# Performance work log

Measured on AMD Instinct MI355X. Metric: run time of the kernel, lower is better.

Reference implementation:

```python
import jax, jax.numpy as jnp
import numpy as np

BIG = 1e8  # > max possible squared distance in a 64^3 volume (3*63^2 ~ 1.2e4)


def _edt(mask):
    """Exact Euclidean distance transform (scipy.ndimage.distance_transform_edt).

    mask: [B, X, Y, Z] float; distance at nonzero voxels to nearest zero voxel.
    Uses the exact separable squared-EDT: along each axis,
      g[i] = min_j f[j] + (i - j)^2  (lower envelope of parabolas, brute-forced).
    """
    f = jnp.where(mask > 0, BIG, 0.0).astype(jnp.float32)
    for ax in (1, 2, 3):
        f = jnp.moveaxis(f, ax, -1)            # [..., n]
        n = f.shape[-1]
        i = jnp.arange(n)
        d2 = ((i[:, None] - i[None, :]) ** 2).astype(jnp.float32)  # [n, n]
        f = jnp.min(f[..., None, :] + d2, axis=-1)                 # [..., n]
        f = jnp.moveaxis(f, -1, ax)
    return jnp.sqrt(f)


def _get_dist_map(mmap, label_inner, label_outer):
    lz = jnp.isin(mmap, jnp.asarray(label_outer)).astype(jnp.float32)
    lz = jnp.where(jnp.isin(mmap, jnp.asarray(label_inner)), 0.0, lz)
    tdm_outer = _edt(lz)                       # distance inside outer region to its zero set
    b = _edt(1.0 - lz)
    boundary = jnp.where(b == 1.0, 1.0, 0.0)   # boundary[boundary != 1] = 0
    outer = tdm_outer + boundary
    level_zero_inner = (outer == 0.0).astype(jnp.float32)
    tsd = -_edt(level_zero_inner) + tdm_outer  # signed distance
    return boundary, tsd


def setup_inputs() -> dict:
    key = jax.random.key(0)
    mmap = jax.random.randint(key, (2, 64, 64, 64), 0, 10, dtype=jnp.int32)
    return {"mmap": mmap}


def reference(mmap):
    d_mean = 2.0
    inner_boundary, phi_inner = _get_dist_map(mmap, [3, 5, 6, 7, 8, 9], [2, 1, 4, 0])
    outer_boundary, phi_outer = _get_dist_map(mmap, [3, 5, 6, 7, 8, 9, 2], [1, 4, 0])
    hausdorff_inner = jnp.abs(inner_boundary * phi_outer)
    hausdorff_outer = jnp.abs(outer_boundary * phi_inner)
    h_in_mean = hausdorff_inner.sum() / inner_boundary.sum()
    h_out_mean = hausdorff_outer.sum() / outer_boundary.sum()
    loss = (h_in_mean - d_mean) ** 2 + (h_out_mean - d_mean) ** 2
    return (h_in_mean, hausdorff_inner.max(), h_out_mean, hausdorff_outer.max(), loss)
```

## Files before the change

### kernel.cpp

```cpp
#include <hip/hip_runtime.h>
#include <math.h>

#define N 64
#define PLANE 4096
#define FBIG 3.4e38f
#define MASK1 0x17u
#define MASK2 0x13u
typedef unsigned long long ull;

#define PART_OFF ((size_t)131072)
#define CTR_OFF (PART_OFF + (size_t)256 * 8 * 4)

__global__ __launch_bounds__(512) void build_bits(const int* __restrict__ mmap,
                                                  void* __restrict__ wsv) {
  __shared__ unsigned char colb[2][8][64];
  const int bid = blockIdx.x;
  const int b = bid >> 6, x = bid & 63;
  const int t = threadIdx.x;
  const int z = t & 63, c = t >> 6;
  const size_t pb = (size_t)(b * N + x) * PLANE;
  unsigned b1 = 0, b2 = 0;
  #pragma unroll
  for (int k = 0; k < 8; ++k) {
    const int v = mmap[pb + (8 * c + k) * N + z];
    b1 |= ((MASK1 >> v) & 1u) << k;
    b2 |= ((MASK2 >> v) & 1u) << k;
  }
  colb[0][c][z] = (unsigned char)b1;
  colb[1][c][z] = (unsigned char)b2;
  __syncthreads();
  if (t < 128) {
    const int mm = t >> 6, zz = t & 63;
    ull v = 0;
    #pragma unroll
    for (int cc = 0; cc < 8; ++cc)
      v |= (ull)colb[mm][cc][zz] << (8 * cc);
    ((ull*)wsv)[((size_t)(mm * 2 + b) * 64 + x) * 64 + zz] = v;
  }
}

__global__ __launch_bounds__(512) void edt_all(void* __restrict__ wsv,
                                               float* __restrict__ out) {
  __shared__ unsigned int g1p[64][65];
  __shared__ float g2T[64][65];
  __shared__ float g2L[64][65];
  __shared__ unsigned char bndB[4096];
  __shared__ float redS[8], redB[8], redM[8];
  __shared__ int lastFlag;
  const int bid = blockIdx.x;
  const int m = bid >> 7;
  const int y0 = bid & 63;
  const int t = threadIdx.x;

  const ull* cxO = (const ull*)wsv + ((size_t)(bid >> 6) & 3) * 4096;
  const ull* cxP = (const ull*)wsv + (size_t)(((1 - m) * 2) + ((bid >> 6) & 1)) * 4096;

  #pragma unroll
  for (int k = 0; k < 8; ++k) {
    const int ci = t + 512 * k;
    const int x = ci >> 6, z = ci & 63;
    const ull c0 = cxO[ci];
    const ull xm = (x > 0) ? cxO[ci - 64] : 0ull;
    const ull xp = (x < 63) ? cxO[ci + 64] : 0ull;
    const ull zm = (z > 0) ? cxO[ci - 1] : 0ull;
    const ull zp = (z < 63) ? cxO[ci + 1] : 0ull;
    const ull mT = ~c0;
    const ull nb = xm | xp | zm | zp | (c0 << 1) | (c0 >> 1);
    const ull mL = c0 | nb;
    const int zs = z * z;
    unsigned vT, vL;
    {
      const ull hi = mT >> y0;
      const int du = hi ? (__ffsll((long long)hi) - 1) : 99;
      const int dd = (int)__clzll((long long)(mT << (63 - y0)));
      const int d = min(du, dd);
      vT = (d > 63) ? 65535u : (unsigned)(d * d + zs);
    }
    {
      const ull hi = mL >> y0;
      const int du = hi ? (__ffsll((long long)hi) - 1) : 99;
      const int dd = (int)__clzll((long long)(mL << (63 - y0)));
      const int d = min(du, dd);
      vL = (d > 63) ? 65535u : (unsigned)(d * d + zs);
    }
    g1p[x][z] = vT | (vL << 16);
    const ull p0 = cxP[ci];
    const ull pxm = (x > 0) ? cxP[ci - 64] : 0ull;
    const ull pxp = (x < 63) ? cxP[ci + 64] : 0ull;
    const ull pzm = (z > 0) ? cxP[ci - 1] : 0ull;
    const ull pzp = (z < 63) ? cxP[ci + 1] : 0ull;
    const ull pnb = pxm | pxp | pzm | pzp | (p0 << 1) | (p0 >> 1);
    bndB[ci] = (unsigned char)(((pnb & ~p0) >> y0) & 1ull);
  }
  __syncthreads();

  {
    const int x = t >> 3, g = t & 7;
    float aT[8], aL[8], zq[8];
    #pragma unroll
    for (int q = 0; q < 8; ++q) {
      aT[q] = FBIG; aL[q] = FBIG; zq[q] = (float)(g + 8 * q);
    }
    const unsigned* row = &g1p[x][0];
    float m2j = 0.f;
    #pragma unroll 4
    for (int j = 0; j < 64; ++j) {
      const unsigned v = row[j];
      const float fT = (float)(v & 0xffffu);
      const float fL = (float)(v >> 16);
      #pragma unroll
      for (int q = 0; q < 8; ++q) {
        aT[q] = fminf(aT[q], fmaf(m2j, zq[q], fT));
        aL[q] = fminf(aL[q], fmaf(m2j, zq[q], fL));
      }
      m2j -= 2.f;
    }
    const float xs = (float)(x * x);
    #pragma unroll
    for (int q = 0; q < 8; ++q) {
      const int zi = g + 8 * q;
      const float z2 = zq[q] * zq[q];
      g2T[x][zi] = aT[q] + z2 + xs;
      g2L[x][zi] = aL[q] + z2 + xs;
    }
  }
  __syncthreads();

  {
    const int z = t >> 3, g = t & 7;
    float aT[8], aL[8], xq[8];
    #pragma unroll
    for (int q = 0; q < 8; ++q) {
      aT[q] = FBIG; aL[q] = FBIG; xq[q] = (float)(g + 8 * q);
    }
    float m2j = 0.f;
    #pragma unroll 4
    for (int j = 0; j < 64; ++j) {
      const float f1 = g2T[j][z];
      const float f2 = g2L[j][z];
      #pragma unroll
      for (int q = 0; q < 8; ++q) {
        aT[q] = fminf(aT[q], fmaf(m2j, xq[q], f1));
        aL[q] = fminf(aL[q], fmaf(m2j, xq[q], f2));
      }
      m2j -= 2.f;
    }
    float hsum = 0.f, bsum = 0.f, hmax = 0.f;
    #pragma unroll
    for (int q = 0; q < 8; ++q) {
      const int x = g + 8 * q;
      const float eT = fmaf(xq[q], xq[q], aT[q]);
      const float eL = fmaf(xq[q], xq[q], aL[q]);
      const float tsd = sqrtf(eT) - sqrtf(eL);
      const float bnd = (float)bndB[x * 64 + z];
      const float h = bnd * fabsf(tsd);
      hsum += h; bsum += bnd; hmax = fmaxf(hmax, h);
    }
    #pragma unroll
    for (int o = 32; o > 0; o >>= 1) {
      hsum += __shfl_down(hsum, o);
      bsum += __shfl_down(bsum, o);
      hmax = fmaxf(hmax, __shfl_down(hmax, o));
    }
    const int w = t >> 6;
    if ((t & 63) == 0) { redS[w] = hsum; redB[w] = bsum; redM[w] = hmax; }
  }
  __syncthreads();

  float* part = (float*)((char*)wsv + PART_OFF);
  int* ctr = (int*)((char*)wsv + CTR_OFF);
  if (t == 0) {
    float s = 0.f, bs = 0.f, mx = 0.f;
    #pragma unroll
    for (int i = 0; i < 8; ++i) {
      s += redS[i]; bs += redB[i]; mx = fmaxf(mx, redM[i]);
    }
    float* p = part + (size_t)bid * 8;
    p[0] = s; p[1] = bs; p[2] = mx;
    __threadfence();
    const int old = atomicAdd(ctr, 1);
    lastFlag = (old == 255) ? 1 : 0;
  }
  __syncthreads();
  if (lastFlag) {
    __threadfence();
    float s = 0.f, bs = 0.f, mx = 0.f;
    if (t < 256) {
      const float* p = part + (size_t)t * 8;
      s = p[0]; bs = p[1]; mx = p[2];
    }
    #pragma unroll
    for (int o = 32; o > 0; o >>= 1) {
      s += __shfl_down(s, o);
      bs += __shfl_down(bs, o);
      mx = fmaxf(mx, __shfl_down(mx, o));
    }
    __syncthreads();
    if ((t & 63) == 0 && t < 256) {
      redS[t >> 6] = s; redB[t >> 6] = bs; redM[t >> 6] = mx;
    }
    __syncthreads();
    if (t == 0) {
      const float s_ho = redS[0] + redS[1], b2 = redB[0] + redB[1];
      const float mho = fmaxf(redM[0], redM[1]);
      const float s_hi = redS[2] + redS[3], b1 = redB[2] + redB[3];
      const float mhi = fmaxf(redM[2], redM[3]);
      const float him = s_hi / b1;
      const float hom = s_ho / b2;
      out[0] = him;
      out[1] = mhi;
      out[2] = hom;
      out[3] = mho;
      out[4] = (him - 2.f) * (him - 2.f) + (hom - 2.f) * (hom - 2.f);
    }
  }
}

extern "C" void kernel_launch(void* const* d_in, const int* in_sizes, int n_in,
                              void* d_out, int out_size, void* d_ws,
                              size_t ws_size, hipStream_t stream) {
  (void)in_sizes; (void)n_in; (void)out_size; (void)ws_size;
  const int* mmap = (const int*)d_in[0];
  float* out = (float*)d_out;

  hipMemsetAsync((char*)d_ws + CTR_OFF, 0, 8, stream);
  build_bits<<<128, 512, 0, stream>>>(mmap, d_ws);
  edt_all<<<256, 512, 0, stream>>>(d_ws, out);
}
```

Baseline: 37.32 us.

## Precompute stencil masks in separate kernel, pack second pass, use 1024-thread blocks

Adds a stencil kernel that computes the dilated mask and boundary bitmasks once per volume instead of recomputing them in every y-slice block. The second EDT pass now stores packed 16-bit T/L values in a transposed shared array read with 128-bit vector loads. The main kernel doubles its block size to 1024 threads with 4 outputs per thread, reducing per-thread register work. The trade-off is an extra kernel launch and a clamp to 65535 that relies on distances fitting in 16 bits.

Measured after the change: 40.40 us. 1.08x slower.

```diff
diff --git a/kernel.cpp b/kernel.cpp
--- a/kernel.cpp
+++ b/kernel.cpp
@@ -6,9 +6,14 @@
 #define FBIG 3.4e38f
 #define MASK1 0x17u
 #define MASK2 0x13u
+#define LP 68
 typedef unsigned long long ull;
-
-#define PART_OFF ((size_t)131072)
+typedef __attribute__((ext_vector_type(4))) unsigned int u32x4;
+
+#define CX_OFF ((size_t)0)
+#define ML_OFF ((size_t)131072)
+#define BD_OFF ((size_t)262144)
+#define PART_OFF ((size_t)393216)
 #define CTR_OFF (PART_OFF + (size_t)256 * 8 * 4)
 
 __global__ __launch_bounds__(512) void build_bits(const int* __restrict__ mmap,
@@ -35,38 +40,48 @@
     #pragma unroll
     for (int cc = 0; cc < 8; ++cc)
       v |= (ull)colb[mm][cc][zz] << (8 * cc);
-    ((ull*)wsv)[((size_t)(mm * 2 + b) * 64 + x) * 64 + zz] = v;
-  }
-}
-
-__global__ __launch_bounds__(512) void edt_all(void* __restrict__ wsv,
-                                               float* __restrict__ out) {
-  __shared__ unsigned int g1p[64][65];
-  __shared__ float g2T[64][65];
-  __shared__ float g2L[64][65];
-  __shared__ unsigned char bndB[4096];
-  __shared__ float redS[8], redB[8], redM[8];
+    ((ull*)((char*)wsv + CX_OFF))[(size_t)(mm * 2 + b) * 4096 + x * 64 + zz] = v;
+  }
+}
+
+__global__ __launch_bounds__(512) void stencil_k(void* __restrict__ wsv) {
+  const int idx = blockIdx.x * 512 + threadIdx.x;
+  const int mi = idx >> 12, ci = idx & 4095;
+  const int x = ci >> 6, z = ci & 63;
+  const ull* cx = (const ull*)((char*)wsv + CX_OFF) + (size_t)mi * 4096;
+  const ull c0 = cx[ci];
+  const ull xm = (x > 0) ? cx[ci - 64] : 0ull;
+  const ull xp = (x < 63) ? cx[ci + 64] : 0ull;
+  const ull zm = (z > 0) ? cx[ci - 1] : 0ull;
+  const ull zp = (z < 63) ? cx[ci + 1] : 0ull;
+  const ull nb = xm | xp | zm | zp | (c0 << 1) | (c0 >> 1);
+  ((ull*)((char*)wsv + ML_OFF))[(size_t)mi * 4096 + ci] = c0 | nb;
+  ((ull*)((char*)wsv + BD_OFF))[(size_t)mi * 4096 + ci] = nb & ~c0;
+}
+
+__global__ __launch_bounds__(1024) void edt_all(void* __restrict__ wsv,
+                                                float* __restrict__ out) {
+  __shared__ unsigned int g1p[64][LP];
+  __shared__ unsigned int g2p[64][LP];
+  __shared__ float redS[16], redB[16], redM[16];
   __shared__ int lastFlag;
   const int bid = blockIdx.x;
   const int m = bid >> 7;
+  const int mi = bid >> 6;
   const int y0 = bid & 63;
   const int t = threadIdx.x;
 
-  const ull* cxO = (const ull*)wsv + ((size_t)(bid >> 6) & 3) * 4096;
-  const ull* cxP = (const ull*)wsv + (size_t)(((1 - m) * 2) + ((bid >> 6) & 1)) * 4096;
+  const ull* cxO = (const ull*)((char*)wsv + CX_OFF) + (size_t)mi * 4096;
+  const ull* mLO = (const ull*)((char*)wsv + ML_OFF) + (size_t)mi * 4096;
+  const ull* bndP = (const ull*)((char*)wsv + BD_OFF) +
+                    (size_t)((1 - m) * 2 + (mi & 1)) * 4096;
 
   #pragma unroll
-  for (int k = 0; k < 8; ++k) {
-    const int ci = t + 512 * k;
+  for (int k = 0; k < 4; ++k) {
+    const int ci = t + 1024 * k;
     const int x = ci >> 6, z = ci & 63;
-    const ull c0 = cxO[ci];
-    const ull xm = (x > 0) ? cxO[ci - 64] : 0ull;
-    const ull xp = (x < 63) ? cxO[ci + 64] : 0ull;
-    const ull zm = (z > 0) ? cxO[ci - 1] : 0ull;
-    const ull zp = (z < 63) ? cxO[ci + 1] : 0ull;
-    const ull mT = ~c0;
-    const ull nb = xm | xp | zm | zp | (c0 << 1) | (c0 >> 1);
-    const ull mL = c0 | nb;
+    const ull mT = ~cxO[ci];
+    const ull mLw = mLO[ci];
     const int zs = z * z;
     unsigned vT, vL;
     {
@@ -77,82 +92,85 @@
       vT = (d > 63) ? 65535u : (unsigned)(d * d + zs);
     }
     {
-      const ull hi = mL >> y0;
+      const ull hi = mLw >> y0;
       const int du = hi ? (__ffsll((long long)hi) - 1) : 99;
-      const int dd = (int)__clzll((long long)(mL << (63 - y0)));
+      const int dd = (int)__clzll((long long)(mLw << (63 - y0)));
       const int d = min(du, dd);
       vL = (d > 63) ? 65535u : (unsigned)(d * d + zs);
     }
     g1p[x][z] = vT | (vL << 16);
-    const ull p0 = cxP[ci];
-    const ull pxm = (x > 0) ? cxP[ci - 64] : 0ull;
-    const ull pxp = (x < 63) ? cxP[ci + 64] : 0ull;
-    const ull pzm = (z > 0) ? cxP[ci - 1] : 0ull;
-    const ull pzp = (z < 63) ? cxP[ci + 1] : 0ull;
-    const ull pnb = pxm | pxp | pzm | pzp | (p0 << 1) | (p0 >> 1);
-    bndB[ci] = (unsigned char)(((pnb & ~p0) >> y0) & 1ull);
   }
   __syncthreads();
 
   {
-    const int x = t >> 3, g = t & 7;
-    float aT[8], aL[8], zq[8];
-    #pragma unroll
-    for (int q = 0; q < 8; ++q) {
-      aT[q] = FBIG; aL[q] = FBIG; zq[q] = (float)(g + 8 * q);
-    }
-    const unsigned* row = &g1p[x][0];
+    const int x = t >> 4, g = t & 15;
+    const u32x4* row4 = (const u32x4*)&g1p[x][0];
+    float aT[4], aL[4], zq[4];
+    #pragma unroll
+    for (int q = 0; q < 4; ++q) {
+      aT[q] = FBIG; aL[q] = FBIG; zq[q] = (float)(g + 16 * q);
+    }
     float m2j = 0.f;
     #pragma unroll 4
-    for (int j = 0; j < 64; ++j) {
-      const unsigned v = row[j];
-      const float fT = (float)(v & 0xffffu);
-      const float fL = (float)(v >> 16);
+    for (int j4 = 0; j4 < 16; ++j4) {
+      const u32x4 v4 = row4[j4];
       #pragma unroll
-      for (int q = 0; q < 8; ++q) {
-        aT[q] = fminf(aT[q], fmaf(m2j, zq[q], fT));
-        aL[q] = fminf(aL[q], fmaf(m2j, zq[q], fL));
+      for (int e = 0; e < 4; ++e) {
+        const unsigned v = v4[e];
+        const float fT = (float)(v & 0xffffu);
+        const float fL = (float)(v >> 16);
+        #pragma unroll
+        for (int q = 0; q < 4; ++q) {
+          aT[q] = fminf(aT[q], fmaf(m2j, zq[q], fT));
+          aL[q] = fminf(aL[q], fmaf(m2j, zq[q], fL));
+        }
+        m2j -= 2.f;
       }
-      m2j -= 2.f;
     }
     const float xs = (float)(x * x);
     #pragma unroll
-    for (int q = 0; q < 8; ++q) {
-      const int zi = g + 8 * q;
-      const float z2 = zq[q] * zq[q];
-      g2T[x][zi] = aT[q] + z2 + xs;
-      g2L[x][zi] = aL[q] + z2 + xs;
+    for (int q = 0; q < 4; ++q) {
+      const int zi = g + 16 * q;
+      const float vT = fminf(fmaf(zq[q], zq[q], aT[q]) + xs, 65535.f);
+      const float vL = fminf(fmaf(zq[q], zq[q], aL[q]) + xs, 65535.f);
+      g2p[zi][x] = (unsigned)vT | ((unsigned)vL << 16);
     }
   }
   __syncthreads();
 
   {
-    const int z = t >> 3, g = t & 7;
-    float aT[8], aL[8], xq[8];
-    #pragma unroll
-    for (int q = 0; q < 8; ++q) {
-      aT[q] = FBIG; aL[q] = FBIG; xq[q] = (float)(g + 8 * q);
+    const int z = t >> 4, g = t & 15;
+    const u32x4* row4 = (const u32x4*)&g2p[z][0];
+    float aT[4], aL[4], xq[4];
+    #pragma unroll
+    for (int q = 0; q < 4; ++q) {
+      aT[q] = FBIG; aL[q] = FBIG; xq[q] = (float)(g + 16 * q);
     }
     float m2j = 0.f;
     #pragma unroll 4
-    for (int j = 0; j < 64; ++j) {
-      const float f1 = g2T[j][z];
-      const float f2 = g2L[j][z];
+    for (int j4 = 0; j4 < 16; ++j4) {
+      const u32x4 v4 = row4[j4];
       #pragma unroll
-      for (int q = 0; q < 8; ++q) {
-        aT[q] = fminf(aT[q], fmaf(m2j, xq[q], f1));
-        aL[q] = fminf(aL[q], fmaf(m2j, xq[q], f2));
+      for (int e = 0; e < 4; ++e) {
+        const unsigned v = v4[e];
+        const float fT = (float)(v & 0xffffu);
+        const float fL = (float)(v >> 16);
+        #pragma unroll
+        for (int q = 0; q < 4; ++q) {
+          aT[q] = fminf(aT[q], fmaf(m2j, xq[q], fT));
+          aL[q] = fminf(aL[q], fmaf(m2j, xq[q], fL));
+        }
+        m2j -= 2.f;
       }
-      m2j -= 2.f;
     }
     float hsum = 0.f, bsum = 0.f, hmax = 0.f;
     #pragma unroll
-    for (int q = 0; q < 8; ++q) {
-      const int x = g + 8 * q;
+    for (int q = 0; q < 4; ++q) {
+      const int x = g + 16 * q;
       const float eT = fmaf(xq[q], xq[q], aT[q]);
       const float eL = fmaf(xq[q], xq[q], aL[q]);
       const float tsd = sqrtf(eT) - sqrtf(eL);
-      const float bnd = (float)bndB[x * 64 + z];
+      const float bnd = (float)((bndP[x * 64 + z] >> y0) & 1ull);
       const float h = bnd * fabsf(tsd);
       hsum += h; bsum += bnd; hmax = fmaxf(hmax, h);
     }
@@ -172,7 +190,7 @@
   if (t == 0) {
     float s = 0.f, bs = 0.f, mx = 0.f;
     #pragma unroll
-    for (int i = 0; i < 8; ++i) {
+    for (int i = 0; i < 16; ++i) {
       s += redS[i]; bs += redB[i]; mx = fmaxf(mx, redM[i]);
     }
     float* p = part + (size_t)bid * 8;
@@ -225,5 +243,6 @@
 
   hipMemsetAsync((char*)d_ws + CTR_OFF, 0, 8, stream);
   build_bits<<<128, 512, 0, stream>>>(mmap, d_ws);
-  edt_all<<<256, 512, 0, stream>>>(d_ws, out);
-}
+  stencil_k<<<32, 512, 0, stream>>>(d_ws);
+  edt_all<<<256, 1024, 0, stream>>>(d_ws, out);
+}
```
